# Optimization experiments

Hardware: AMD Instinct MI355X
Metric: run time of the kernel (lower is better)

## Reference

```python
import jax, jax.numpy as jnp
import numpy as np

NEG_SLOPE = 0.01  # torch nn.LeakyReLU default

N_NODES = 100000
N_EDGES = 1000000
D_FEAT = 64


def setup_inputs() -> dict:
    key = jax.random.key(0)
    ks = jax.random.split(key, 8)
    x = jax.random.normal(ks[0], (N_NODES, D_FEAT), dtype=jnp.float32)
    src = jax.random.randint(ks[1], (N_EDGES,), 0, N_NODES, dtype=jnp.int64 if jax.config.jax_enable_x64 else jnp.int32)
    dst = jax.random.randint(ks[2], (N_EDGES,), 0, N_NODES, dtype=jnp.int64 if jax.config.jax_enable_x64 else jnp.int32)
    s = 1.0 / np.sqrt(D_FEAT)
    W1 = jax.random.normal(ks[3], (D_FEAT, 64), dtype=jnp.float32) * s
    b1 = jnp.zeros((64,), dtype=jnp.float32)
    W2 = jax.random.normal(ks[4], (64, 64), dtype=jnp.float32) * s
    b2 = jnp.zeros((64,), dtype=jnp.float32)
    Wc = jax.random.normal(ks[5], (64, 2), dtype=jnp.float32) * s
    bc = jnp.zeros((2,), dtype=jnp.float32)
    return {"x": x, "src": src, "dst": dst, "W1": W1, "b1": b1,
            "W2": W2, "b2": b2, "Wc": Wc, "bc": bc}


def _graph_conv(x, src, dst, W, b, out_deg_isqrt, in_deg_isqrt, n_nodes):
    # DGL GraphConv, norm='both': h_v = ( sum_{u->v} x_u / sqrt(d_out(u)) ) / sqrt(d_in(v)) @ W + b
    # (in_feats <= out_feats here, so aggregate first then transform, matching DGL order)
    h = x * out_deg_isqrt[:, None]          # [N, d] scale by source out-degree
    msg = h[src]                            # [E, d] gather
    agg = jax.ops.segment_sum(msg, dst, num_segments=n_nodes)  # [N, d] scatter-add
    agg = agg * in_deg_isqrt[:, None]
    return agg @ W + b


def reference(x, src, dst, W1, b1, W2, b2, Wc, bc):
    n = x.shape[0]
    ones_e = jnp.ones(src.shape[0], dtype=x.dtype)
    out_deg = jnp.clip(jax.ops.segment_sum(ones_e, src, num_segments=n), 1.0)
    in_deg = jnp.clip(jax.ops.segment_sum(ones_e, dst, num_segments=n), 1.0)
    out_isqrt = out_deg ** -0.5
    in_isqrt = in_deg ** -0.5

    h = _graph_conv(x, src, dst, W1, b1, out_isqrt, in_isqrt, n)
    h = jax.nn.leaky_relu(h, NEG_SLOPE)
    h = _graph_conv(h, src, dst, W2, b2, out_isqrt, in_isqrt, n)
    h = jax.nn.leaky_relu(h, NEG_SLOPE)
    return h @ Wc + bc  # prediction=True -> linear classifier
```

## Files before the change

kernel.cpp:

```cpp
#include <hip/hip_runtime.h>


typedef __attribute__((ext_vector_type(8))) short short8;
typedef __attribute__((ext_vector_type(4))) float f32x4;

#define NPB 256
#define SEG 64
#define BSH 9
#define BW  512

__device__ __forceinline__ float b2f(unsigned short u) {
    return __uint_as_float(((unsigned int)u) << 16);
}
__device__ __forceinline__ unsigned short f2b(float f) {
    unsigned int i = __float_as_uint(f);
    unsigned int r = (i + 0x7FFFu + ((i >> 16) & 1u)) >> 16;
    return (unsigned short)r;
}

__device__ __forceinline__ void acc8(float* a, short8 f) {
    int4 d = *(int4*)&f;
#pragma unroll
    for (int q = 0; q < 4; q++) {
        unsigned int dw = (unsigned int)((q == 0) ? d.x : (q == 1) ? d.y
                                       : (q == 2) ? d.z : d.w);
        a[2 * q]     += __uint_as_float(dw << 16);
        a[2 * q + 1] += __uint_as_float(dw & 0xFFFF0000u);
    }
}

__global__ __launch_bounds__(1024) void count_kernel(
    const int* __restrict__ src, const int* __restrict__ dst,
    int* __restrict__ cntD, int* __restrict__ cntS, int e, int chunk) {
    __shared__ int hD[256], hS[256];
    int t = threadIdx.x, pb = blockIdx.x;
    if (t < 256) { hD[t] = 0; hS[t] = 0; }
    __syncthreads();
    int e0 = pb * chunk, e1 = min(e, e0 + chunk);
    for (int i = e0 + 4 * t; i + 3 < e1; i += 4096) {
        int4 d4 = *(const int4*)(dst + i);
        int4 s4 = *(const int4*)(src + i);
        atomicAdd(&hD[d4.x >> BSH], 1);
        atomicAdd(&hD[d4.y >> BSH], 1);
        atomicAdd(&hD[d4.z >> BSH], 1);
        atomicAdd(&hD[d4.w >> BSH], 1);
        atomicAdd(&hS[s4.x >> BSH], 1);
        atomicAdd(&hS[s4.y >> BSH], 1);
        atomicAdd(&hS[s4.z >> BSH], 1);
        atomicAdd(&hS[s4.w >> BSH], 1);
    }
    int tb0 = e0 + ((e1 - e0) & ~3);
    for (int i = tb0 + t; i < e1; i += 1024) {
        atomicAdd(&hD[dst[i] >> BSH], 1);
        atomicAdd(&hS[src[i] >> BSH], 1);
    }
    __syncthreads();
    if (t < 256) {
        cntD[t * NPB + pb] = hD[t];
        cntS[t * NPB + pb] = hS[t];
    }
}

__global__ __launch_bounds__(1024) void scanmat_kernel(int* __restrict__ cntD,
                                                       int* __restrict__ cntS) {
    int* a = (blockIdx.x == 0) ? cntD : cntS;
    int4* a4 = (int4*)a;
    __shared__ int s[1024];
    int t = threadIdx.x;
    int4 v[SEG / 4];
    int sum = 0;
#pragma unroll
    for (int j = 0; j < SEG / 4; j++) {
        v[j] = a4[t * (SEG / 4) + j];
        sum += v[j].x + v[j].y + v[j].z + v[j].w;
    }
    s[t] = sum;
    __syncthreads();
    for (int d = 1; d < 1024; d <<= 1) {
        int x = (t >= d) ? s[t - d] : 0;
        __syncthreads();
        s[t] += x;
        __syncthreads();
    }
    int run = s[t] - sum;
#pragma unroll
    for (int j = 0; j < SEG / 4; j++) {
        int p0 = run;
        int p1 = p0 + v[j].x;
        int p2 = p1 + v[j].y;
        int p3 = p2 + v[j].z;
        run = p3 + v[j].w;
        a4[t * (SEG / 4) + j] = make_int4(p0, p1, p2, p3);
    }
}

__global__ __launch_bounds__(1024) void part_kernel(
    const int* __restrict__ src, const int* __restrict__ dst,
    const int* __restrict__ cntD, const int* __restrict__ cntS,
    unsigned int* __restrict__ ebuf, unsigned short* __restrict__ sbuf,
    int e, int chunk) {
    __shared__ int cD[256], cS[256];
    int t = threadIdx.x, pb = blockIdx.x;
    if (t < 256) {
        cD[t] = cntD[t * NPB + pb];
        cS[t] = cntS[t * NPB + pb];
    }
    __syncthreads();
    int e0 = pb * chunk, e1 = min(e, e0 + chunk);
    for (int i = e0 + 4 * t; i + 3 < e1; i += 4096) {
        int4 d4 = *(const int4*)(dst + i);
        int4 s4 = *(const int4*)(src + i);
#pragma unroll
        for (int k = 0; k < 4; k++) {
            int s_ = (k == 0) ? s4.x : (k == 1) ? s4.y : (k == 2) ? s4.z : s4.w;
            int d_ = (k == 0) ? d4.x : (k == 1) ? d4.y : (k == 2) ? d4.z : d4.w;
            int pd = atomicAdd(&cD[d_ >> BSH], 1);
            ebuf[pd] = ((unsigned int)s_ << BSH) | (unsigned int)(d_ & (BW - 1));
            int ps_ = atomicAdd(&cS[s_ >> BSH], 1);
            sbuf[ps_] = (unsigned short)(s_ & (BW - 1));
        }
    }
    int tb0 = e0 + ((e1 - e0) & ~3);
    for (int i = tb0 + t; i < e1; i += 1024) {
        int s_ = src[i], d_ = dst[i];
        int pd = atomicAdd(&cD[d_ >> BSH], 1);
        ebuf[pd] = ((unsigned int)s_ << BSH) | (unsigned int)(d_ & (BW - 1));
        int ps_ = atomicAdd(&cS[s_ >> BSH], 1);
        sbuf[ps_] = (unsigned short)(s_ & (BW - 1));
    }
}

__global__ __launch_bounds__(256) void bucket_kernel(
    const unsigned int* __restrict__ ebuf, const unsigned short* __restrict__ sbuf,
    const int* __restrict__ cntD, const int* __restrict__ cntS,
    int* __restrict__ row, int* __restrict__ lenp,
    float* __restrict__ ii, float* __restrict__ oi,
    int* __restrict__ csr, int n, int e) {
    __shared__ int cnt[BW], cur[BW], ocnt[BW], ps[256];
    int t = threadIdx.x, b = blockIdx.x;
    int v0 = b << BSH;
    int eb0 = cntD[b * NPB], eb1 = cntD[(b + 1) * NPB];
    int sb0 = cntS[b * NPB], sb1 = cntS[(b + 1) * NPB];
    int pbase = ((eb0 + 3) & ~3) + (v0 << 2);
    cnt[t] = 0; cnt[t + 256] = 0;
    ocnt[t] = 0; ocnt[t + 256] = 0;
    __syncthreads();
    for (int i = eb0 + t; i < eb1; i += 256)
        atomicAdd(&cnt[ebuf[i] & (BW - 1)], 1);
    for (int i = sb0 + t; i < sb1; i += 256)
        atomicAdd(&ocnt[sbuf[i]], 1);
    __syncthreads();
    int c0 = cnt[2 * t], c1 = cnt[2 * t + 1];
    int p0 = (c0 + 3) & ~3, p1 = (c1 + 3) & ~3;
    int ppair = p0 + p1;
    ps[t] = ppair;
    __syncthreads();
    for (int d = 1; d < 256; d <<= 1) {
        int x = (t >= d) ? ps[t - d] : 0;
        __syncthreads();
        ps[t] += x;
        __syncthreads();
    }
    int pexcl = ps[t] - ppair;
    cur[2 * t] = pexcl;
    cur[2 * t + 1] = pexcl + p0;
    int v = v0 + 2 * t;
    if (v < n) {
        row[v] = pbase + pexcl;
        lenp[v] = p0;
        ii[v] = rsqrtf((float)max(c0, 1));
    }
    if (v + 1 < n) {
        row[v + 1] = pbase + pexcl + p0;
        lenp[v + 1] = p1;
        ii[v + 1] = rsqrtf((float)max(c1, 1));
    }
    for (int j = t; j < BW; j += 256) {
        int vv = v0 + j;
        if (vv < n) oi[vv] = rsqrtf((float)max(ocnt[j], 1));
    }
    __syncthreads();
    for (int i = eb0 + t; i < eb1; i += 256) {
        unsigned int p = ebuf[i];
        int r = atomicAdd(&cur[p & (BW - 1)], 1);
        csr[pbase + r] = (int)(p >> BSH);
    }
    if (v < n)
        for (int k = c0; k < p0; k++) csr[pbase + pexcl + k] = n;
    if (v + 1 < n)
        for (int k = c1; k < p1; k++) csr[pbase + pexcl + p0 + k] = n;
}

__global__ __launch_bounds__(256) void xconv_kernel(
    const float4* __restrict__ x4, const float* __restrict__ oi,
    ushort4* __restrict__ xb, ushort4* __restrict__ h1b4, int total4) {
    int idx = blockIdx.x * blockDim.x + threadIdx.x;
    int stride = gridDim.x * blockDim.x;
    for (int i = idx; i < total4; i += stride) {
        float s = oi[i >> 4];
        float4 val = x4[i];
        xb[i] = make_ushort4(f2b(val.x * s), f2b(val.y * s),
                             f2b(val.z * s), f2b(val.w * s));
    }
    if (idx < 16) {
        xb[total4 + idx] = make_ushort4(0, 0, 0, 0);
        h1b4[total4 + idx] = make_ushort4(0, 0, 0, 0);
    }
}

template <bool FINAL>
__global__ __launch_bounds__(256) void fused_kernel(
    const short8* __restrict__ featb, const int* __restrict__ row,
    const int* __restrict__ lenp, const int* __restrict__ csr,
    const float* __restrict__ ii, const float* __restrict__ oi,
    const float* __restrict__ W, const float* __restrict__ bias,
    const float* __restrict__ Wc, const float* __restrict__ bcl,
    void* __restrict__ out, int n, int nwaves) {
    __shared__ short8 tile[4][16 * 9];
    int lane = threadIdx.x & 63;
    int o = lane >> 3, s = lane & 7;
    int m15 = lane & 15, quad = lane >> 4;
    short8* tl = tile[threadIdx.x >> 6];
    int wid = blockIdx.x * (blockDim.x >> 6) + (threadIdx.x >> 6);
    int ngroups = (n + 15) >> 4;

    short8 bf[4][2];
#pragma unroll
    for (int nt = 0; nt < 4; nt++)
#pragma unroll
        for (int kk = 0; kk < 2; kk++)
#pragma unroll
            for (int j = 0; j < 8; j++)
                bf[nt][kk][j] = (short)f2b(W[(kk * 32 + quad * 8 + j) * 64 + nt * 16 + m15]);

    float bias_r[4];
#pragma unroll
    for (int nt = 0; nt < 4; nt++) bias_r[nt] = bias[nt * 16 + m15];

    float wc_r[4][2];
    float bc0 = 0.f, bc1 = 0.f;
    if constexpr (FINAL) {
#pragma unroll
        for (int nt = 0; nt < 4; nt++) {
            wc_r[nt][0] = Wc[(nt * 16 + m15) * 2];
            wc_r[nt][1] = Wc[(nt * 16 + m15) * 2 + 1];
        }
        bc0 = bcl[0];
        bc1 = bcl[1];
    }

    for (int g = wid; g < ngroups; g += nwaves) {
        int rbase = g << 4;

#pragma unroll
        for (int p = 0; p < 2; p++) {
            int v = rbase + p * 8 + o;
            bool valid = v < n;
            int base = 0, pc = 0;
            if (valid) { base = row[v]; pc = lenp[v]; }
            float a[8];
#pragma unroll
            for (int k = 0; k < 8; k++) a[k] = 0.f;
            int j = 0;
            for (; j + 7 < pc; j += 8) {
                int4 u0 = *(const int4*)(csr + base + j);
                int4 u1 = *(const int4*)(csr + base + j + 4);
                short8 f0 = featb[(size_t)u0.x * 8 + s];
                short8 f1 = featb[(size_t)u0.y * 8 + s];
                short8 f2 = featb[(size_t)u0.z * 8 + s];
                short8 f3 = featb[(size_t)u0.w * 8 + s];
                short8 f4 = featb[(size_t)u1.x * 8 + s];
                short8 f5 = featb[(size_t)u1.y * 8 + s];
                short8 f6 = featb[(size_t)u1.z * 8 + s];
                short8 f7 = featb[(size_t)u1.w * 8 + s];
                acc8(a, f0); acc8(a, f1); acc8(a, f2); acc8(a, f3);
                acc8(a, f4); acc8(a, f5); acc8(a, f6); acc8(a, f7);
            }
            if (j < pc) {
                int4 u0 = *(const int4*)(csr + base + j);
                short8 f0 = featb[(size_t)u0.x * 8 + s];
                short8 f1 = featb[(size_t)u0.y * 8 + s];
                short8 f2 = featb[(size_t)u0.z * 8 + s];
                short8 f3 = featb[(size_t)u0.w * 8 + s];
                acc8(a, f0); acc8(a, f1); acc8(a, f2); acc8(a, f3);
            }
            float iiv = valid ? ii[v] : 0.f;
            short8 r;
#pragma unroll
            for (int m = 0; m < 8; m++) r[m] = (short)f2b(a[m] * iiv);
            tl[(p * 8 + o) * 9 + s] = r;
        }

        short8 af0 = tl[m15 * 9 + quad];
        short8 af1 = tl[m15 * 9 + 4 + quad];

        f32x4 acc[4];
#pragma unroll
        for (int nt = 0; nt < 4; nt++) {
            f32x4 z = {0.f, 0.f, 0.f, 0.f};
            z = __builtin_amdgcn_mfma_f32_16x16x32_bf16(af0, bf[nt][0], z, 0, 0, 0);
            z = __builtin_amdgcn_mfma_f32_16x16x32_bf16(af1, bf[nt][1], z, 0, 0, 0);
            acc[nt] = z;
        }

        if constexpr (!FINAL) {
#pragma unroll
            for (int r = 0; r < 4; r++) {
                int vr = rbase + quad * 4 + r;
                float os = (vr < n) ? oi[vr] : 0.f;
#pragma unroll
                for (int nt = 0; nt < 4; nt++) {
                    float ov = acc[nt][r] + bias_r[nt];
                    ov = (ov > 0.f) ? ov : 0.01f * ov;
                    if (vr < n)
                        ((unsigned short*)out)[(size_t)vr * 64 + nt * 16 + m15] = f2b(ov * os);
                }
            }
        } else {
#pragma unroll
            for (int r = 0; r < 4; r++) {
                float p0 = 0.f, p1 = 0.f;
#pragma unroll
                for (int nt = 0; nt < 4; nt++) {
                    float ov = acc[nt][r] + bias_r[nt];
                    ov = (ov > 0.f) ? ov : 0.01f * ov;
                    p0 = fmaf(ov, wc_r[nt][0], p0);
                    p1 = fmaf(ov, wc_r[nt][1], p1);
                }
#pragma unroll
                for (int off = 1; off < 16; off <<= 1) {
                    p0 += __shfl_xor(p0, off);
                    p1 += __shfl_xor(p1, off);
                }
                int vr = rbase + quad * 4 + r;
                if (m15 == 0 && vr < n)
                    ((float2*)out)[vr] = make_float2(p0 + bc0, p1 + bc1);
            }
        }
    }
}

extern "C" void kernel_launch(void* const* d_in, const int* in_sizes, int n_in,
                              void* d_out, int out_size, void* d_ws, size_t ws_size,
                              hipStream_t stream) {
    const float* x  = (const float*)d_in[0];
    const int* src  = (const int*)d_in[1];
    const int* dst  = (const int*)d_in[2];
    const float* W1 = (const float*)d_in[3];
    const float* b1 = (const float*)d_in[4];
    const float* W2 = (const float*)d_in[5];
    const float* b2 = (const float*)d_in[6];
    const float* Wc = (const float*)d_in[7];
    const float* bc = (const float*)d_in[8];
    int n = in_sizes[0] / 64;
    int e = in_sizes[1];
    int total = n * 64;
    int nbuck = (n + BW - 1) >> BSH;

    char* ws = (char*)d_ws;
    size_t off = 0;
    auto take = [&](size_t bytes) -> char* {
        char* p = ws + off;
        off = (off + bytes + 255) & ~(size_t)255;
        return p;
    };
    int* cntD = (int*)take(256 * NPB * 4);
    int* cntS = (int*)take(256 * NPB * 4);
    unsigned int* ebuf = (unsigned int*)take((size_t)e * 4);
    unsigned short* sbuf = (unsigned short*)take((size_t)e * 2);
    int* row  = (int*)take((size_t)(n + 1) * 4);
    int* lenp = (int*)take((size_t)n * 4);
    int* csr  = (int*)take(((size_t)e + 4 * (size_t)nbuck * BW + 16) * 4);
    float* oi = (float*)take((size_t)n * 4);
    float* ii = (float*)take((size_t)n * 4);
    unsigned short* xb  = (unsigned short*)take((size_t)(total + 64) * 2);
    unsigned short* h1b = (unsigned short*)take((size_t)(total + 64) * 2);

    int chunk = (((e + NPB - 1) / NPB) + 3) & ~3;

    count_kernel<<<NPB, 1024, 0, stream>>>(src, dst, cntD, cntS, e, chunk);
    scanmat_kernel<<<2, 1024, 0, stream>>>(cntD, cntS);
    part_kernel<<<NPB, 1024, 0, stream>>>(src, dst, cntD, cntS, ebuf, sbuf, e, chunk);
    bucket_kernel<<<nbuck, 256, 0, stream>>>(ebuf, sbuf, cntD, cntS,
                                             row, lenp, ii, oi, csr, n, e);
    xconv_kernel<<<2048, 256, 0, stream>>>((const float4*)x, oi, (ushort4*)xb,
                                           (ushort4*)h1b, n * 16);

    const int fblocks = 1568;
    const int fwaves = fblocks * (256 / 64);

    fused_kernel<false><<<fblocks, 256, 0, stream>>>((const short8*)xb, row, lenp, csr,
                                                     ii, oi, W1, b1, nullptr, nullptr,
                                                     h1b, n, fwaves);
    fused_kernel<true><<<fblocks, 256, 0, stream>>>((const short8*)h1b, row, lenp, csr,
                                                    ii, nullptr, W2, b2, Wc, bc,
                                                    d_out, n, fwaves);
}
```

Before: 196.8 us.

## Pad CSR rows to 8 and interleave two destination rows' gathers

The CSR build now pads each destination row to a multiple of 8 instead of 4, and the bucket kernel runs 512 threads with one node per thread. The gather loop in the fused kernel now processes both of a lane's destination rows at once, issuing up to 16 independent feature loads per iteration. The aim is more memory-level parallelism to hide gather latency. In exchange, the extra padding adds dummy loads of the zero row (average degree is about 10), and register pressure rises from holding 16 short8 values.

```diff
diff --git a/kernel.cpp b/kernel.cpp
--- a/kernel.cpp
+++ b/kernel.cpp
@@ -130,65 +130,52 @@
     }
 }
 
-__global__ __launch_bounds__(256) void bucket_kernel(
+__global__ __launch_bounds__(512) void bucket_kernel(
     const unsigned int* __restrict__ ebuf, const unsigned short* __restrict__ sbuf,
     const int* __restrict__ cntD, const int* __restrict__ cntS,
     int* __restrict__ row, int* __restrict__ lenp,
     float* __restrict__ ii, float* __restrict__ oi,
     int* __restrict__ csr, int n, int e) {
-    __shared__ int cnt[BW], cur[BW], ocnt[BW], ps[256];
+    __shared__ int cnt[BW], cur[BW], ocnt[BW], ps[BW];
     int t = threadIdx.x, b = blockIdx.x;
     int v0 = b << BSH;
     int eb0 = cntD[b * NPB], eb1 = cntD[(b + 1) * NPB];
     int sb0 = cntS[b * NPB], sb1 = cntS[(b + 1) * NPB];
-    int pbase = ((eb0 + 3) & ~3) + (v0 << 2);
-    cnt[t] = 0; cnt[t + 256] = 0;
-    ocnt[t] = 0; ocnt[t + 256] = 0;
-    __syncthreads();
-    for (int i = eb0 + t; i < eb1; i += 256)
+    int pbase = ((eb0 + 7) & ~7) + (v0 << 3);
+    cnt[t] = 0; ocnt[t] = 0;
+    __syncthreads();
+    for (int i = eb0 + t; i < eb1; i += 512)
         atomicAdd(&cnt[ebuf[i] & (BW - 1)], 1);
-    for (int i = sb0 + t; i < sb1; i += 256)
+    for (int i = sb0 + t; i < sb1; i += 512)
         atomicAdd(&ocnt[sbuf[i]], 1);
     __syncthreads();
-    int c0 = cnt[2 * t], c1 = cnt[2 * t + 1];
-    int p0 = (c0 + 3) & ~3, p1 = (c1 + 3) & ~3;
-    int ppair = p0 + p1;
-    ps[t] = ppair;
-    __syncthreads();
-    for (int d = 1; d < 256; d <<= 1) {
+    int c = cnt[t];
+    int p = (c + 7) & ~7;
+    ps[t] = p;
+    __syncthreads();
+    for (int d = 1; d < 512; d <<= 1) {
         int x = (t >= d) ? ps[t - d] : 0;
         __syncthreads();
         ps[t] += x;
         __syncthreads();
     }
-    int pexcl = ps[t] - ppair;
-    cur[2 * t] = pexcl;
-    cur[2 * t + 1] = pexcl + p0;
-    int v = v0 + 2 * t;
+    int pexcl = ps[t] - p;
+    cur[t] = pexcl;
+    int v = v0 + t;
     if (v < n) {
         row[v] = pbase + pexcl;
-        lenp[v] = p0;
-        ii[v] = rsqrtf((float)max(c0, 1));
-    }
-    if (v + 1 < n) {
-        row[v + 1] = pbase + pexcl + p0;
-        lenp[v + 1] = p1;
-        ii[v + 1] = rsqrtf((float)max(c1, 1));
-    }
-    for (int j = t; j < BW; j += 256) {
-        int vv = v0 + j;
-        if (vv < n) oi[vv] = rsqrtf((float)max(ocnt[j], 1));
-    }
-    __syncthreads();
-    for (int i = eb0 + t; i < eb1; i += 256) {
-        unsigned int p = ebuf[i];
-        int r = atomicAdd(&cur[p & (BW - 1)], 1);
-        csr[pbase + r] = (int)(p >> BSH);
+        lenp[v] = p;
+        ii[v] = rsqrtf((float)max(c, 1));
+        oi[v] = rsqrtf((float)max(ocnt[t], 1));
+    }
+    __syncthreads();
+    for (int i = eb0 + t; i < eb1; i += 512) {
+        unsigned int pk = ebuf[i];
+        int r = atomicAdd(&cur[pk & (BW - 1)], 1);
+        csr[pbase + r] = (int)(pk >> BSH);
     }
     if (v < n)
-        for (int k = c0; k < p0; k++) csr[pbase + pexcl + k] = n;
-    if (v + 1 < n)
-        for (int k = c1; k < p1; k++) csr[pbase + pexcl + p0 + k] = n;
+        for (int k = c; k < p; k++) csr[pbase + pexcl + k] = n;
 }
 
 __global__ __launch_bounds__(256) void xconv_kernel(
@@ -252,44 +239,69 @@
     for (int g = wid; g < ngroups; g += nwaves) {
         int rbase = g << 4;
 
-#pragma unroll
-        for (int p = 0; p < 2; p++) {
-            int v = rbase + p * 8 + o;
-            bool valid = v < n;
-            int base = 0, pc = 0;
-            if (valid) { base = row[v]; pc = lenp[v]; }
-            float a[8];
-#pragma unroll
-            for (int k = 0; k < 8; k++) a[k] = 0.f;
-            int j = 0;
-            for (; j + 7 < pc; j += 8) {
-                int4 u0 = *(const int4*)(csr + base + j);
-                int4 u1 = *(const int4*)(csr + base + j + 4);
-                short8 f0 = featb[(size_t)u0.x * 8 + s];
-                short8 f1 = featb[(size_t)u0.y * 8 + s];
-                short8 f2 = featb[(size_t)u0.z * 8 + s];
-                short8 f3 = featb[(size_t)u0.w * 8 + s];
-                short8 f4 = featb[(size_t)u1.x * 8 + s];
-                short8 f5 = featb[(size_t)u1.y * 8 + s];
-                short8 f6 = featb[(size_t)u1.z * 8 + s];
-                short8 f7 = featb[(size_t)u1.w * 8 + s];
-                acc8(a, f0); acc8(a, f1); acc8(a, f2); acc8(a, f3);
-                acc8(a, f4); acc8(a, f5); acc8(a, f6); acc8(a, f7);
-            }
-            if (j < pc) {
-                int4 u0 = *(const int4*)(csr + base + j);
-                short8 f0 = featb[(size_t)u0.x * 8 + s];
-                short8 f1 = featb[(size_t)u0.y * 8 + s];
-                short8 f2 = featb[(size_t)u0.z * 8 + s];
-                short8 f3 = featb[(size_t)u0.w * 8 + s];
-                acc8(a, f0); acc8(a, f1); acc8(a, f2); acc8(a, f3);
-            }
-            float iiv = valid ? ii[v] : 0.f;
-            short8 r;
-#pragma unroll
-            for (int m = 0; m < 8; m++) r[m] = (short)f2b(a[m] * iiv);
-            tl[(p * 8 + o) * 9 + s] = r;
-        }
+        int vA = rbase + o, vB = rbase + 8 + o;
+        bool valA = vA < n, valB = vB < n;
+        int baseA = 0, pcA = 0, baseB = 0, pcB = 0;
+        if (valA) { baseA = row[vA]; pcA = lenp[vA]; }
+        if (valB) { baseB = row[vB]; pcB = lenp[vB]; }
+        float aA[8], aB[8];
+#pragma unroll
+        for (int k = 0; k < 8; k++) { aA[k] = 0.f; aB[k] = 0.f; }
+        int jA = 0, jB = 0;
+        while (jA < pcA || jB < pcB) {
+            bool dA = jA < pcA, dB = jB < pcB;
+            int4 uA0, uA1, uB0, uB1;
+            short8 fA0, fA1, fA2, fA3, fA4, fA5, fA6, fA7;
+            short8 fB0, fB1, fB2, fB3, fB4, fB5, fB6, fB7;
+            if (dA) {
+                uA0 = *(const int4*)(csr + baseA + jA);
+                uA1 = *(const int4*)(csr + baseA + jA + 4);
+            }
+            if (dB) {
+                uB0 = *(const int4*)(csr + baseB + jB);
+                uB1 = *(const int4*)(csr + baseB + jB + 4);
+            }
+            if (dA) {
+                fA0 = featb[(size_t)uA0.x * 8 + s];
+                fA1 = featb[(size_t)uA0.y * 8 + s];
+                fA2 = featb[(size_t)uA0.z * 8 + s];
+                fA3 = featb[(size_t)uA0.w * 8 + s];
+                fA4 = featb[(size_t)uA1.x * 8 + s];
+                fA5 = featb[(size_t)uA1.y * 8 + s];
+                fA6 = featb[(size_t)uA1.z * 8 + s];
+                fA7 = featb[(size_t)uA1.w * 8 + s];
+            }
+            if (dB) {
+                fB0 = featb[(size_t)uB0.x * 8 + s];
+                fB1 = featb[(size_t)uB0.y * 8 + s];
+                fB2 = featb[(size_t)uB0.z * 8 + s];
+                fB3 = featb[(size_t)uB0.w * 8 + s];
+                fB4 = featb[(size_t)uB1.x * 8 + s];
+                fB5 = featb[(size_t)uB1.y * 8 + s];
+                fB6 = featb[(size_t)uB1.z * 8 + s];
+                fB7 = featb[(size_t)uB1.w * 8 + s];
+            }
+            if (dA) {
+                acc8(aA, fA0); acc8(aA, fA1); acc8(aA, fA2); acc8(aA, fA3);
+                acc8(aA, fA4); acc8(aA, fA5); acc8(aA, fA6); acc8(aA, fA7);
+                jA += 8;
+            }
+            if (dB) {
+                acc8(aB, fB0); acc8(aB, fB1); acc8(aB, fB2); acc8(aB, fB3);
+                acc8(aB, fB4); acc8(aB, fB5); acc8(aB, fB6); acc8(aB, fB7);
+                jB += 8;
+            }
+        }
+        float iivA = valA ? ii[vA] : 0.f;
+        float iivB = valB ? ii[vB] : 0.f;
+        short8 rA, rB;
+#pragma unroll
+        for (int m = 0; m < 8; m++) {
+            rA[m] = (short)f2b(aA[m] * iivA);
+            rB[m] = (short)f2b(aB[m] * iivB);
+        }
+        tl[o * 9 + s] = rA;
+        tl[(8 + o) * 9 + s] = rB;
 
         short8 af0 = tl[m15 * 9 + quad];
         short8 af1 = tl[m15 * 9 + 4 + quad];
@@ -370,7 +382,7 @@
     unsigned short* sbuf = (unsigned short*)take((size_t)e * 2);
     int* row  = (int*)take((size_t)(n + 1) * 4);
     int* lenp = (int*)take((size_t)n * 4);
-    int* csr  = (int*)take(((size_t)e + 4 * (size_t)nbuck * BW + 16) * 4);
+    int* csr  = (int*)take(((size_t)e + 8 * (size_t)nbuck * BW + 16) * 4);
     float* oi = (float*)take((size_t)n * 4);
     float* ii = (float*)take((size_t)n * 4);
     unsigned short* xb  = (unsigned short*)take((size_t)(total + 64) * 2);
@@ -381,7 +393,7 @@
     count_kernel<<<NPB, 1024, 0, stream>>>(src, dst, cntD, cntS, e, chunk);
     scanmat_kernel<<<2, 1024, 0, stream>>>(cntD, cntS);
     part_kernel<<<NPB, 1024, 0, stream>>>(src, dst, cntD, cntS, ebuf, sbuf, e, chunk);
-    bucket_kernel<<<nbuck, 256, 0, stream>>>(ebuf, sbuf, cntD, cntS,
+    bucket_kernel<<<nbuck, 512, 0, stream>>>(ebuf, sbuf, cntD, cntS,
                                              row, lenp, ii, oi, csr, n, e);
     xconv_kernel<<<2048, 256, 0, stream>>>((const float4*)x, oi, (ushort4*)xb,
                                            (ushort4*)h1b, n * 16);
```

Result: slower. 203.4 us (+3.4%).
